# Kernel optimization log

Measured on AMD Instinct MI355X. Metric: run time of the kernel, lower is better.

The kernel has to match this reference:

```python
import math
import jax, jax.numpy as jnp
import numpy as np

R = 4096      # number of hex regions (nodes)
D = 64        # feature dim d
DEG = 6       # hex degree
E = R * DEG   # edges
M_REG = 8     # Fourier frequency bank size
FB_ALPHA = 0.1
MAX_EXP = 80.0   # mah clamp: mah <= MAX_EXP / 0.5
EPS_DIV = 1e-12


def setup_inputs() -> dict:
    key = jax.random.key(0)
    ks = jax.random.split(key, 8)
    # ring-lattice degree-6 adjacency standing in for the hex graph
    offsets = np.array([-3, -2, -1, 1, 2, 3], dtype=np.int64)
    src = ((np.arange(R, dtype=np.int64)[:, None] + offsets[None, :]) % R).reshape(-1)
    dst = np.repeat(np.arange(R, dtype=np.int64), DEG)
    # axial-style integer grid coordinates, used as floats
    idx = np.arange(R)
    coords = np.stack([idx % 64, idx // 64], axis=-1).astype(np.float32)
    return {
        "H": jax.random.normal(ks[0], (R, D), dtype=jnp.float32),
        "reg_mask_prev": jnp.ones((R,), dtype=bool),
        "reg_coords": jnp.asarray(coords),
        "W_edge": 0.02 * jax.random.normal(ks[1], (E, D, D), dtype=jnp.float32),
        "key_W": 0.02 * jax.random.normal(ks[2], (E, D, D), dtype=jnp.float32),
        "raw_P_edge": jnp.zeros((E, D), dtype=jnp.float32),
        "query_W": 0.02 * jax.random.normal(ks[3], (R, D, D), dtype=jnp.float32),
        "W_reg": jax.random.normal(ks[4], (M_REG, 2), dtype=jnp.float32),  # gaussian freq bank, sigma=1
        "beta_cos": 0.01 * jax.random.normal(ks[5], (M_REG,), dtype=jnp.float32),
        "beta_sin": 0.01 * jax.random.normal(ks[6], (M_REG,), dtype=jnp.float32),
        "src_idx": jnp.asarray(src),
        "dst_idx": jnp.asarray(dst),
    }


def reference(H, reg_mask_prev, reg_coords, W_edge, key_W, raw_P_edge, query_W,
              W_reg, beta_cos, beta_sin, src_idx, dst_idx) -> jnp.ndarray:
    R_, D_ = H.shape
    fb_scale = 1.0 / math.sqrt(W_reg.shape[0])
    edge_mask = reg_mask_prev[src_idx]                       # [E]
    H_src = H[src_idx]                                       # [E, d] gather
    H_dst = H[dst_idx]                                       # [E, d]
    # per-edge linear transform (torch.bmm over stacked W_edge weights)
    msg = jnp.einsum("eij,ej->ei", W_edge, H_src)            # [E, d]
    # multiplicative Fourier relative-position bias
    delta = reg_coords[dst_idx] - reg_coords[src_idx]        # [E, 2]
    S = delta @ W_reg.T                                      # [E, m]
    b = (jnp.cos(S) * beta_cos + jnp.sin(S) * beta_sin).sum(-1) * fb_scale  # [E]
    msg = msg * (1.0 + FB_ALPHA * b)[:, None]
    # content scores: per-node query, per-edge key
    q = jnp.einsum("rij,rj->ri", query_W, H)                 # [R, d]
    K = jnp.einsum("eij,ej->ei", key_W, H_src)               # [E, d]
    scores = (q[dst_idx] * K).sum(-1) / math.sqrt(D_)        # [E]
    # robust (Mahalanobis) term
    P_edge = jax.nn.softplus(raw_P_edge)                     # [E, d]
    resid = msg - H_dst
    mah = jnp.minimum((resid * resid * P_edge).sum(-1), MAX_EXP / 0.5)
    logw = scores - 0.5 * mah                                # [E]
    logw = jnp.where(edge_mask, logw, -jnp.inf)
    # per-destination segment softmax (stable)
    max_logw = jax.ops.segment_max(logw, dst_idx, num_segments=R_)
    ex = jnp.where(edge_mask, jnp.exp(logw - max_logw[dst_idx]), 0.0)
    exp_sum = jax.ops.segment_sum(ex, dst_idx, num_segments=R_)
    logZ = max_logw + jnp.log(jnp.maximum(exp_sum, EPS_DIV))
    w = jnp.where(edge_mask, jnp.exp(logw - logZ[dst_idx]), 0.0)  # [E]
    # scatter-add weighted messages
    M = jax.ops.segment_sum(w[:, None] * msg, dst_idx, num_segments=R_)  # [R, d]
    return M
```

## Files before the change

### kernel.cpp

```cpp
#include <hip/hip_runtime.h>
#include <cmath>


#define R_N   4096
#define D_N   64
#define DEG_N 6

__device__ __forceinline__ float softplusf(float x) {
    return (x > 20.0f) ? x : log1pf(expf(x));
}

__global__ __launch_bounds__(256) void router_kernel(
    const float* __restrict__ H,
    const int*   __restrict__ mask,
    const float* __restrict__ coords,
    const float* __restrict__ W_edge,
    const float* __restrict__ key_W,
    const float* __restrict__ rawP,
    const float* __restrict__ query_W,
    const float* __restrict__ W_reg,
    const float* __restrict__ beta_cos,
    const float* __restrict__ beta_sin,
    const int*   __restrict__ src_idx,
    float*       __restrict__ out)
{
    const int r    = blockIdx.x;
    const int t    = threadIdx.x;
    const int wave = t >> 6;
    const int lane = t & 63;

    __shared__ float hdst[64];
    __shared__ float hsrc[DEG_N][64];
    __shared__ float qv[64];
    __shared__ float msg[DEG_N][64];
    __shared__ float sc_part[DEG_N][4];
    __shared__ float mahs[DEG_N];
    __shared__ float bfr[DEG_N];
    __shared__ int   smask[DEG_N];
    __shared__ float wgt[DEG_N];

    if (t < 64) hdst[t] = H[(size_t)r * 64 + t];
    for (int idx = t; idx < DEG_N * 64; idx += 256) {
        int k = idx >> 6, d = idx & 63;
        int s = src_idx[r * DEG_N + k];
        hsrc[k][d] = H[(size_t)s * 64 + d];
    }
    if (t < DEG_N) {
        int s = src_idx[r * DEG_N + t];
        smask[t] = (mask[s] != 0);
        float dx = coords[2 * r + 0] - coords[2 * s + 0];
        float dy = coords[2 * r + 1] - coords[2 * s + 1];
        float b = 0.f;
        #pragma unroll
        for (int m = 0; m < 8; ++m) {
            float S = dx * W_reg[2 * m + 0] + dy * W_reg[2 * m + 1];
            b += cosf(S) * beta_cos[m] + sinf(S) * beta_sin[m];
        }
        bfr[t] = 1.0f + 0.1f * b * 0.35355339059327373f;
    }
    __syncthreads();

    const int row = t >> 2;
    const int c0  = (t & 3) * 16;

    {
        const float4* wp = reinterpret_cast<const float4*>(
            query_W + (size_t)r * 4096 + (size_t)t * 16);
        float4 w0 = wp[0], w1 = wp[1], w2 = wp[2], w3 = wp[3];
        const float* x = hdst + c0;
        float a = w0.x*x[0]  + w0.y*x[1]  + w0.z*x[2]  + w0.w*x[3]
                + w1.x*x[4]  + w1.y*x[5]  + w1.z*x[6]  + w1.w*x[7]
                + w2.x*x[8]  + w2.y*x[9]  + w2.z*x[10] + w2.w*x[11]
                + w3.x*x[12] + w3.y*x[13] + w3.z*x[14] + w3.w*x[15];
        a += __shfl_xor(a, 1);
        a += __shfl_xor(a, 2);
        if ((t & 3) == 0) qv[row] = a;
    }
    __syncthreads();

    const float qrow = qv[row];

    for (int k = 0; k < DEG_N; ++k) {
        const size_t e = (size_t)r * DEG_N + k;
        const float4* wp = reinterpret_cast<const float4*>(
            W_edge + e * 4096 + (size_t)t * 16);
        const float4* kp = reinterpret_cast<const float4*>(
            key_W + e * 4096 + (size_t)t * 16);
        float4 a0 = wp[0], a1 = wp[1], a2 = wp[2], a3 = wp[3];
        float4 b0 = kp[0], b1 = kp[1], b2 = kp[2], b3 = kp[3];
        const float* x = hsrc[k] + c0;

        float am = a0.x*x[0]  + a0.y*x[1]  + a0.z*x[2]  + a0.w*x[3]
                 + a1.x*x[4]  + a1.y*x[5]  + a1.z*x[6]  + a1.w*x[7]
                 + a2.x*x[8]  + a2.y*x[9]  + a2.z*x[10] + a2.w*x[11]
                 + a3.x*x[12] + a3.y*x[13] + a3.z*x[14] + a3.w*x[15];
        float ak = b0.x*x[0]  + b0.y*x[1]  + b0.z*x[2]  + b0.w*x[3]
                 + b1.x*x[4]  + b1.y*x[5]  + b1.z*x[6]  + b1.w*x[7]
                 + b2.x*x[8]  + b2.y*x[9]  + b2.z*x[10] + b2.w*x[11]
                 + b3.x*x[12] + b3.y*x[13] + b3.z*x[14] + b3.w*x[15];

        am += __shfl_xor(am, 1);
        am += __shfl_xor(am, 2);
        if ((t & 3) == 0) msg[k][row] = am * bfr[k];

        float c = ak * qrow;
        #pragma unroll
        for (int s2 = 1; s2 < 64; s2 <<= 1) c += __shfl_xor(c, s2);
        if (lane == 0) sc_part[k][wave] = c;
    }
    __syncthreads();

    for (int k = wave; k < DEG_N; k += 4) {
        float m = msg[k][lane] - hdst[lane];
        float p = softplusf(rawP[((size_t)r * DEG_N + k) * 64 + lane]);
        float c = m * m * p;
        #pragma unroll
        for (int s2 = 1; s2 < 64; s2 <<= 1) c += __shfl_xor(c, s2);
        if (lane == 0) mahs[k] = c;
    }
    __syncthreads();

    if (t == 0) {
        float lw[DEG_N];
        float maxl = -INFINITY;
        #pragma unroll
        for (int k = 0; k < DEG_N; ++k) {
            float sc = (sc_part[k][0] + sc_part[k][1] +
                        sc_part[k][2] + sc_part[k][3]) * 0.125f;
            float mh = fminf(mahs[k], 160.0f);
            float l  = smask[k] ? (sc - 0.5f * mh) : -INFINITY;
            lw[k] = l;
            maxl  = fmaxf(maxl, l);
        }
        float s = 0.f;
        #pragma unroll
        for (int k = 0; k < DEG_N; ++k)
            s += smask[k] ? expf(lw[k] - maxl) : 0.f;
        float logZ = maxl + logf(fmaxf(s, 1e-12f));
        #pragma unroll
        for (int k = 0; k < DEG_N; ++k)
            wgt[k] = smask[k] ? expf(lw[k] - logZ) : 0.f;
    }
    __syncthreads();

    if (t < 64) {
        float o = 0.f;
        #pragma unroll
        for (int k = 0; k < DEG_N; ++k) o += wgt[k] * msg[k][t];
        out[(size_t)r * 64 + t] = o;
    }
}

extern "C" void kernel_launch(void* const* d_in, const int* in_sizes, int n_in,
                              void* d_out, int out_size, void* d_ws, size_t ws_size,
                              hipStream_t stream) {
    const float* H        = (const float*)d_in[0];
    const int*   mask     = (const int*)  d_in[1];
    const float* coords   = (const float*)d_in[2];
    const float* W_edge   = (const float*)d_in[3];
    const float* key_W    = (const float*)d_in[4];
    const float* rawP     = (const float*)d_in[5];
    const float* query_W  = (const float*)d_in[6];
    const float* W_reg    = (const float*)d_in[7];
    const float* bcos     = (const float*)d_in[8];
    const float* bsin     = (const float*)d_in[9];
    const int*   src      = (const int*)  d_in[10];

    float* out = (float*)d_out;
    router_kernel<<<R_N, 256, 0, stream>>>(
        H, mask, coords, W_edge, key_W, rawP, query_W,
        W_reg, bcos, bsin, src, out);
}
```

Measured before the change: 153.2 us.

## Vectorize prologue loads, prefetch rawP, defer score reduction, unroll edge loop

The prologue now loads H rows, the destination row and the rawP rows into shared memory with float4 loads spread across disjoint thread groups. Full K vectors are stored to shared memory, and the score dot product is done after the loop together with the Mahalanobis reduction. This removes one barrier and the per-edge 64-wide shuffle reduction from the edge loop. The edge loop is fully unrolled so the loads for all six edges can be issued early, which raises register pressure and adds shared-memory traffic.

```diff
diff --git a/kernel.cpp b/kernel.cpp
--- a/kernel.cpp
+++ b/kernel.cpp
@@ -3,7 +3,6 @@
 
 
 #define R_N   4096
-#define D_N   64
 #define DEG_N 6
 
 __device__ __forceinline__ float softplusf(float x) {
@@ -31,23 +30,34 @@
 
     __shared__ float hdst[64];
     __shared__ float hsrc[DEG_N][64];
+    __shared__ float pls[DEG_N][64];
     __shared__ float qv[64];
     __shared__ float msg[DEG_N][64];
-    __shared__ float sc_part[DEG_N][4];
+    __shared__ float kk[DEG_N][64];
+    __shared__ float scs[DEG_N];
     __shared__ float mahs[DEG_N];
     __shared__ float bfr[DEG_N];
     __shared__ int   smask[DEG_N];
     __shared__ float wgt[DEG_N];
 
-    if (t < 64) hdst[t] = H[(size_t)r * 64 + t];
-    for (int idx = t; idx < DEG_N * 64; idx += 256) {
-        int k = idx >> 6, d = idx & 63;
+    if (t < 96) {
+        int k = t >> 4, j = t & 15;
         int s = src_idx[r * DEG_N + k];
-        hsrc[k][d] = H[(size_t)s * 64 + d];
-    }
-    if (t < DEG_N) {
-        int s = src_idx[r * DEG_N + t];
-        smask[t] = (mask[s] != 0);
+        reinterpret_cast<float4*>(&hsrc[k][0])[j] =
+            reinterpret_cast<const float4*>(H + (size_t)s * 64)[j];
+    } else if (t < 192) {
+        int u = t - 96;
+        int k = u >> 4, j = u & 15;
+        reinterpret_cast<float4*>(&pls[k][0])[j] =
+            reinterpret_cast<const float4*>(rawP + ((size_t)r * DEG_N + k) * 64)[j];
+    } else if (t < 208) {
+        int j = t - 192;
+        reinterpret_cast<float4*>(&hdst[0])[j] =
+            reinterpret_cast<const float4*>(H + (size_t)r * 64)[j];
+    } else if (t < 208 + DEG_N) {
+        int k = t - 208;
+        int s = src_idx[r * DEG_N + k];
+        smask[k] = (mask[s] != 0);
         float dx = coords[2 * r + 0] - coords[2 * s + 0];
         float dy = coords[2 * r + 1] - coords[2 * s + 1];
         float b = 0.f;
@@ -56,7 +66,7 @@
             float S = dx * W_reg[2 * m + 0] + dy * W_reg[2 * m + 1];
             b += cosf(S) * beta_cos[m] + sinf(S) * beta_sin[m];
         }
-        bfr[t] = 1.0f + 0.1f * b * 0.35355339059327373f;
+        bfr[k] = 1.0f + 0.1f * b * 0.35355339059327373f;
     }
     __syncthreads();
 
@@ -65,7 +75,7 @@
 
     {
         const float4* wp = reinterpret_cast<const float4*>(
-            query_W + (size_t)r * 4096 + (size_t)t * 16);
+            query_W + (size_t)r * 4096) + t * 4;
         float4 w0 = wp[0], w1 = wp[1], w2 = wp[2], w3 = wp[3];
         const float* x = hdst + c0;
         float a = w0.x*x[0]  + w0.y*x[1]  + w0.z*x[2]  + w0.w*x[3]
@@ -76,16 +86,15 @@
         a += __shfl_xor(a, 2);
         if ((t & 3) == 0) qv[row] = a;
     }
-    __syncthreads();
 
-    const float qrow = qv[row];
-
+    const float4* wbase = reinterpret_cast<const float4*>(
+        W_edge + (size_t)r * DEG_N * 4096) + t * 4;
+    const float4* kbase = reinterpret_cast<const float4*>(
+        key_W + (size_t)r * DEG_N * 4096) + t * 4;
+    #pragma unroll
     for (int k = 0; k < DEG_N; ++k) {
-        const size_t e = (size_t)r * DEG_N + k;
-        const float4* wp = reinterpret_cast<const float4*>(
-            W_edge + e * 4096 + (size_t)t * 16);
-        const float4* kp = reinterpret_cast<const float4*>(
-            key_W + e * 4096 + (size_t)t * 16);
+        const float4* wp = wbase + k * 1024;
+        const float4* kp = kbase + k * 1024;
         float4 a0 = wp[0], a1 = wp[1], a2 = wp[2], a3 = wp[3];
         float4 b0 = kp[0], b1 = kp[1], b2 = kp[2], b3 = kp[3];
         const float* x = hsrc[k] + c0;
@@ -101,22 +110,29 @@
 
         am += __shfl_xor(am, 1);
         am += __shfl_xor(am, 2);
-        if ((t & 3) == 0) msg[k][row] = am * bfr[k];
-
-        float c = ak * qrow;
-        #pragma unroll
-        for (int s2 = 1; s2 < 64; s2 <<= 1) c += __shfl_xor(c, s2);
-        if (lane == 0) sc_part[k][wave] = c;
+        ak += __shfl_xor(ak, 1);
+        ak += __shfl_xor(ak, 2);
+        if ((t & 3) == 0) {
+            msg[k][row] = am * bfr[k];
+            kk[k][row]  = ak;
+        }
     }
     __syncthreads();
 
     for (int k = wave; k < DEG_N; k += 4) {
+        float c = kk[k][lane] * qv[lane];
         float m = msg[k][lane] - hdst[lane];
-        float p = softplusf(rawP[((size_t)r * DEG_N + k) * 64 + lane]);
-        float c = m * m * p;
+        float p = softplusf(pls[k][lane]);
+        float g = m * m * p;
         #pragma unroll
-        for (int s2 = 1; s2 < 64; s2 <<= 1) c += __shfl_xor(c, s2);
-        if (lane == 0) mahs[k] = c;
+        for (int s2 = 1; s2 < 64; s2 <<= 1) {
+            c += __shfl_xor(c, s2);
+            g += __shfl_xor(g, s2);
+        }
+        if (lane == 0) {
+            scs[k]  = c * 0.125f;
+            mahs[k] = g;
+        }
     }
     __syncthreads();
 
@@ -125,10 +141,8 @@
         float maxl = -INFINITY;
         #pragma unroll
         for (int k = 0; k < DEG_N; ++k) {
-            float sc = (sc_part[k][0] + sc_part[k][1] +
-                        sc_part[k][2] + sc_part[k][3]) * 0.125f;
             float mh = fminf(mahs[k], 160.0f);
-            float l  = smask[k] ? (sc - 0.5f * mh) : -INFINITY;
+            float l  = smask[k] ? (scs[k] - 0.5f * mh) : -INFINITY;
             lw[k] = l;
             maxl  = fmaxf(maxl, l);
         }
```

Result: slower. 160.5 us (+4.7%).
